# Kernel optimization log

Measured on AMD Instinct MI355X. Metric: run time of the kernel, lower is better.

The kernel has to match this reference:

```python
import jax, jax.numpy as jnp
import numpy as np

N_NODES = 50000
N_EDGES = 800000
IN_DIM = 1200   # latent_size * num_heads
OUT_DIM = 300
NEG_SLOPE = 0.2  # PyG GATConv default


def setup_inputs() -> dict:
    key = jax.random.key(0)
    k1, k2, k3, k4, k5 = jax.random.split(key, 5)
    z = jax.random.normal(k1, (N_NODES, IN_DIM), dtype=jnp.float32)
    edge_index = jax.random.randint(k2, (2, N_EDGES), 0, N_NODES, dtype=jnp.int64)
    # GATConv params (heads=1): lin weight [out, in], attention vectors [out], bias [out]
    W = jax.random.normal(k3, (OUT_DIM, IN_DIM), dtype=jnp.float32) * (1.0 / np.sqrt(IN_DIM))
    att_src = jax.random.normal(k4, (OUT_DIM,), dtype=jnp.float32) * 0.1
    att_dst = jax.random.normal(k5, (OUT_DIM,), dtype=jnp.float32) * 0.1
    bias = jnp.zeros((OUT_DIM,), dtype=jnp.float32)
    return {"z": z, "edge_index": edge_index, "W": W,
            "att_src": att_src, "att_dst": att_dst, "bias": bias}


def reference(z, edge_index, W, att_src, att_dst, bias):
    N = z.shape[0]
    # Linear projection (no bias on lin in GATConv; bias added after aggregation)
    x = z @ W.T                                   # [N, OUT_DIM]
    # add self-loops (GATConv default add_self_loops=True)
    loop = jnp.arange(N, dtype=edge_index.dtype)
    src = jnp.concatenate([edge_index[0], loop])  # message source j
    dst = jnp.concatenate([edge_index[1], loop])  # message target i
    # per-node attention logits
    a_src = x @ att_src                           # [N]
    a_dst = x @ att_dst                           # [N]
    # per-edge score, softmax over incoming edges of each target node
    e = jax.nn.leaky_relu(a_src[src] + a_dst[dst], negative_slope=NEG_SLOPE)  # [E+N]
    e_max = jax.ops.segment_max(e, dst, num_segments=N)   # every node has a self-loop
    ex = jnp.exp(e - e_max[dst])
    denom = jax.ops.segment_sum(ex, dst, num_segments=N)
    alpha = ex / denom[dst]                       # [E+N]
    # weighted aggregation (scatter-add over targets)
    out = jax.ops.segment_sum(alpha[:, None] * x[src], dst, num_segments=N)
    return out + bias
```

## Files before the change

kernel.cpp:

```cpp
#include <hip/hip_runtime.h>

#define N_NODES 50000
#define N_EDGES 800000
#define IN_DIM  1200
#define KP      1216
#define OUT_DIM 300
#define BNP     320
#define XBS     304
#define NSLOTS  (N_EDGES + N_NODES)
#define BM      96
#define GRID_M  ((N_NODES + BM - 1) / BM)

typedef __attribute__((ext_vector_type(8))) short short8;
typedef __attribute__((ext_vector_type(4))) float f32x4;

__device__ __forceinline__ short f2bf(float f) {
  unsigned u = __builtin_bit_cast(unsigned, f);
  u += 0x7fffu + ((u >> 16) & 1u);
  return (short)(u >> 16);
}
__device__ __forceinline__ float bf2f(unsigned short h) {
  return __builtin_bit_cast(float, (unsigned)h << 16);
}
__device__ __forceinline__ float lrelu(float v) { return v > 0.f ? v : 0.2f * v; }

__device__ __forceinline__ float wredMaxF(float v) {
  #pragma unroll
  for (int o = 32; o > 0; o >>= 1) v = fmaxf(v, __shfl_xor(v, o));
  return v;
}
__device__ __forceinline__ float wredSumF(float v) {
  #pragma unroll
  for (int o = 32; o > 0; o >>= 1) v += __shfl_xor(v, o);
  return v;
}

__global__ __launch_bounds__(256) void wconv(const float* __restrict__ W,
                                             unsigned short* __restrict__ Wb) {
  int f = blockIdx.x * 256 + threadIdx.x;
  if (f >= BNP * KP / 8) return;
  int n = (f * 8) / KP, c = (f * 8) % KP;
  short8 v = {0,0,0,0,0,0,0,0};
  if (n < OUT_DIM && c < IN_DIM) {
    const float4* p = reinterpret_cast<const float4*>(W + (size_t)n * IN_DIM + c);
    float4 f0 = p[0], f1 = p[1];
    v[0]=f2bf(f0.x); v[1]=f2bf(f0.y); v[2]=f2bf(f0.z); v[3]=f2bf(f0.w);
    v[4]=f2bf(f1.x); v[5]=f2bf(f1.y); v[6]=f2bf(f1.z); v[7]=f2bf(f1.w);
  }
  *reinterpret_cast<short8*>(&Wb[(size_t)n * KP + c]) = v;
}

__global__ __launch_bounds__(256, 2) void gemm_x(const float* __restrict__ z,
                                                 const unsigned short* __restrict__ Wb,
                                                 const float* __restrict__ att_s,
                                                 const float* __restrict__ att_d,
                                                 unsigned short* __restrict__ xb,
                                                 float* __restrict__ a_s,
                                                 float* __restrict__ a_d) {
  __shared__ unsigned short As[BM * 64];

  const int tid  = threadIdx.x;
  const int lane = tid & 63;
  const int wid  = tid >> 6;
  const int lr   = lane & 15;
  const int lg   = lane >> 4;
  const int m0   = blockIdx.x * BM;

  f32x4 zero4 = {0.f, 0.f, 0.f, 0.f};
  const float4 fz4 = make_float4(0.f, 0.f, 0.f, 0.f);
  f32x4 acc[6][5];
  #pragma unroll
  for (int mf = 0; mf < 6; ++mf)
    #pragma unroll
    for (int nj = 0; nj < 5; ++nj) acc[mf][nj] = zero4;

  const unsigned short* bp = Wb + (size_t)(80 * wid + lr) * KP + lg * 8;

  float4 st[3][2];
  const int srow[3] = { (tid + 0)   >> 3, (tid + 256) >> 3, (tid + 512) >> 3 };
  const int sch [3] = { (tid + 0)   & 7,  (tid + 256) & 7,  (tid + 512) & 7  };

  #define LOADST(KT)                                                          \
    _Pragma("unroll")                                                         \
    for (int j = 0; j < 3; ++j) {                                             \
      int m = m0 + srow[j], k = (KT) * 64 + sch[j] * 8;                       \
      if (m < N_NODES && k < IN_DIM) {                                        \
        const float4* p = reinterpret_cast<const float4*>(z + (size_t)m * IN_DIM + k); \
        st[j][0] = p[0]; st[j][1] = p[1];                                     \
      } else { st[j][0] = fz4; st[j][1] = fz4; }                              \
    }

  LOADST(0);

  for (int kt = 0; kt < 19; ++kt) {
    __syncthreads();
    #pragma unroll
    for (int j = 0; j < 3; ++j) {
      short8 v;
      v[0]=f2bf(st[j][0].x); v[1]=f2bf(st[j][0].y); v[2]=f2bf(st[j][0].z); v[3]=f2bf(st[j][0].w);
      v[4]=f2bf(st[j][1].x); v[5]=f2bf(st[j][1].y); v[6]=f2bf(st[j][1].z); v[7]=f2bf(st[j][1].w);
      int c2 = sch[j] ^ (srow[j] & 7);
      *reinterpret_cast<short8*>(&As[srow[j] * 64 + c2 * 8]) = v;
    }
    __syncthreads();
    if (kt < 18) { LOADST(kt + 1) }

    const unsigned short* bpk = bp + kt * 64;
    short8 bfr[5][2];
    #pragma unroll
    for (int nj = 0; nj < 5; ++nj) {
      bfr[nj][0] = *reinterpret_cast<const short8*>(bpk + (size_t)nj * 16 * KP);
      bfr[nj][1] = *reinterpret_cast<const short8*>(bpk + (size_t)nj * 16 * KP + 32);
    }

    const int sw = lr & 7;
    #pragma unroll
    for (int mf = 0; mf < 6; ++mf) {
      int arow = mf * 16 + lr;
      short8 a0 = *reinterpret_cast<const short8*>(&As[arow * 64 + ((lg    ) ^ sw) * 8]);
      short8 a1 = *reinterpret_cast<const short8*>(&As[arow * 64 + ((4 + lg) ^ sw) * 8]);
      #pragma unroll
      for (int nj = 0; nj < 5; ++nj) {
        acc[mf][nj] = __builtin_amdgcn_mfma_f32_16x16x32_bf16(a0, bfr[nj][0], acc[mf][nj], 0, 0, 0);
        acc[mf][nj] = __builtin_amdgcn_mfma_f32_16x16x32_bf16(a1, bfr[nj][1], acc[mf][nj], 0, 0, 0);
      }
    }
  }
  #undef LOADST

  __syncthreads();
  float* red = reinterpret_cast<float*>(As);

  float vs[5], vd[5];
  #pragma unroll
  for (int nj = 0; nj < 5; ++nj) {
    int c = 80 * wid + 16 * nj + lr;
    bool cv = c < OUT_DIM;
    vs[nj] = cv ? att_s[c] : 0.f;
    vd[nj] = cv ? att_d[c] : 0.f;
  }

  #pragma unroll
  for (int mf = 0; mf < 6; ++mf) {
    float ps[4] = {0.f,0.f,0.f,0.f}, pd[4] = {0.f,0.f,0.f,0.f};
    #pragma unroll
    for (int nj = 0; nj < 5; ++nj) {
      int c = 80 * wid + 16 * nj + lr;
      bool cv = c < OUT_DIM;
      #pragma unroll
      for (int jj = 0; jj < 4; ++jj) {
        float val = acc[mf][nj][jj];
        int r = m0 + 16 * mf + 4 * lg + jj;
        if (cv && r < N_NODES) xb[(size_t)r * XBS + c] = (unsigned short)f2bf(val);
        ps[jj] += val * vs[nj];
        pd[jj] += val * vd[nj];
      }
    }
    #pragma unroll
    for (int jj = 0; jj < 4; ++jj) {
      #pragma unroll
      for (int o = 8; o > 0; o >>= 1) {
        ps[jj] += __shfl_xor(ps[jj], o);
        pd[jj] += __shfl_xor(pd[jj], o);
      }
    }
    if (lr == 0) {
      #pragma unroll
      for (int jj = 0; jj < 4; ++jj) {
        int rr = 16 * mf + 4 * lg + jj;
        red[wid * 96 + rr]       = ps[jj];
        red[384 + wid * 96 + rr] = pd[jj];
      }
    }
  }
  __syncthreads();
  if (tid < 96) {
    int r = m0 + tid;
    if (r < N_NODES)
      a_s[r] = red[tid] + red[96 + tid] + red[192 + tid] + red[288 + tid];
  } else if (tid < 192) {
    int t = tid - 96, r = m0 + t;
    if (r < N_NODES)
      a_d[r] = red[384 + t] + red[384 + 96 + t] + red[384 + 192 + t] + red[384 + 288 + t];
  }
}

__global__ void hist(const int* __restrict__ ei, int* __restrict__ deg) {
  int e = blockIdx.x * blockDim.x + threadIdx.x;
  if (e < N_EDGES) {
    unsigned dst = (unsigned)ei[N_EDGES + e];
    if (dst < N_NODES) atomicAdd(&deg[dst], 1);
  }
}

#define SCAN_B 1024
#define NBLK   49

__global__ __launch_bounds__(SCAN_B) void scan1(const int* __restrict__ deg,
                                                int* __restrict__ bsum) {
  int i = blockIdx.x * SCAN_B + threadIdx.x;
  int v = (i < N_NODES) ? deg[i] + 1 : 0;
  #pragma unroll
  for (int o = 32; o > 0; o >>= 1) v += __shfl_xor(v, o);
  __shared__ int wt[16];
  if ((threadIdx.x & 63) == 0) wt[threadIdx.x >> 6] = v;
  __syncthreads();
  if (threadIdx.x == 0) {
    int t = 0;
    #pragma unroll
    for (int w = 0; w < 16; ++w) t += wt[w];
    bsum[blockIdx.x] = t;
  }
}

__global__ void scan2(const int* __restrict__ bsum, int* __restrict__ bex,
                      int* __restrict__ offs) {
  int l = threadIdx.x;
  int v = (l < NBLK) ? bsum[l] : 0;
  int incl = v;
  #pragma unroll
  for (int off = 1; off < 64; off <<= 1) {
    int u = __shfl_up(incl, off);
    if (l >= off) incl += u;
  }
  if (l < NBLK) bex[l] = incl - v;
  if (l == NBLK - 1) offs[N_NODES] = incl;
}

__global__ __launch_bounds__(SCAN_B) void scan3(const int* __restrict__ deg,
                                                const int* __restrict__ bex,
                                                int* __restrict__ offs,
                                                int* __restrict__ cursor) {
  int tid = threadIdx.x;
  int i = blockIdx.x * SCAN_B + tid;
  int lane = tid & 63, wid = tid >> 6;
  int v = (i < N_NODES) ? deg[i] + 1 : 0;
  int incl = v;
  #pragma unroll
  for (int off = 1; off < 64; off <<= 1) {
    int u = __shfl_up(incl, off);
    if (lane >= off) incl += u;
  }
  __shared__ int wt[16];
  if (lane == 63) wt[wid] = incl;
  __syncthreads();
  if (tid < 16) {
    int t = wt[tid];
    int sc = t;
    #pragma unroll
    for (int off = 1; off < 16; off <<= 1) {
      int u = __shfl_up(sc, off);
      if (tid >= off) sc += u;
    }
    wt[tid] = sc - t;
  }
  __syncthreads();
  int excl = incl - v + wt[wid] + bex[blockIdx.x];
  if (i < N_NODES) { offs[i] = excl; cursor[i] = excl; }
}

__global__ void fill(const int* __restrict__ ei, int* __restrict__ cursor,
                     int* __restrict__ srcs) {
  int e = blockIdx.x * blockDim.x + threadIdx.x;
  if (e < N_EDGES) {
    unsigned dst = (unsigned)ei[N_EDGES + e];
    unsigned src = (unsigned)ei[e];
    if (dst < N_NODES && src < N_NODES) {
      int pos = atomicAdd(&cursor[dst], 1);
      srcs[pos] = (int)src;
    }
  }
}

__global__ __launch_bounds__(256) void weights(const float* __restrict__ a_s,
                                               const float* __restrict__ a_d,
                                               const int* __restrict__ offs,
                                               const int* __restrict__ srcs,
                                               int2* __restrict__ packed) {
  int node = blockIdx.x * 4 + (threadIdx.x >> 6);
  if (node >= N_NODES) return;
  int lane = threadIdx.x & 63;
  int beg = offs[node], end = offs[node + 1];
  int ne = end - 1 - beg;
  float adi = a_d[node];
  float eself = lrelu(a_s[node] + adi);

  float m = eself;
  for (int k = lane; k < ne; k += 64)
    m = fmaxf(m, lrelu(a_s[srcs[beg + k]] + adi));
  m = wredMaxF(m);

  float s = 0.f;
  for (int k = lane; k < ne; k += 64)
    s += expf(lrelu(a_s[srcs[beg + k]] + adi) - m);
  s = wredSumF(s) + expf(eself - m);
  float inv = 1.0f / s;

  for (int k = lane; k < ne; k += 64) {
    int sj = srcs[beg + k];
    float w = expf(lrelu(a_s[sj] + adi) - m) * inv;
    packed[beg + k] = make_int2(sj, __float_as_int(w));
  }
  if (lane == 0)
    packed[end - 1] = make_int2(node, __float_as_int(expf(eself - m) * inv));
}

#define CCH 15
__global__ __launch_bounds__(256) void aggregate(const unsigned short* __restrict__ xb,
                                                 const int2* __restrict__ packed,
                                                 const int* __restrict__ offs,
                                                 const float* __restrict__ bias,
                                                 float* __restrict__ out) {
  unsigned wi = blockIdx.x * 256u + threadIdx.x;
  if (wi >= (unsigned)N_NODES * CCH) return;
  unsigned node = wi / CCH;
  unsigned cc = wi - node * CCH;

  int beg = offs[node], end = offs[node + 1];
  const unsigned short* xcol = xb + 20u * cc;

  float acc[20];
  #pragma unroll
  for (int q = 0; q < 20; ++q) acc[q] = 0.f;

  for (int k = beg; k < end; ++k) {
    int2 pw = packed[k];
    float w = __builtin_bit_cast(float, pw.y);
    const unsigned short* xr = xcol + (size_t)pw.x * XBS;
    #pragma unroll
    for (int q = 0; q < 5; ++q) {
      ushort4 xv = *reinterpret_cast<const ushort4*>(xr + 4 * q);
      acc[4*q+0] += w * bf2f(xv.x);
      acc[4*q+1] += w * bf2f(xv.y);
      acc[4*q+2] += w * bf2f(xv.z);
      acc[4*q+3] += w * bf2f(xv.w);
    }
  }
  float* op = out + (size_t)node * OUT_DIM + 20u * cc;
  const float* bp = bias + 20u * cc;
  #pragma unroll
  for (int q = 0; q < 5; ++q) {
    float4 b = *reinterpret_cast<const float4*>(bp + 4 * q);
    float4 o = {acc[4*q] + b.x, acc[4*q+1] + b.y, acc[4*q+2] + b.z, acc[4*q+3] + b.w};
    *reinterpret_cast<float4*>(op + 4 * q) = o;
  }
}

extern "C" void kernel_launch(void* const* d_in, const int* in_sizes, int n_in,
                              void* d_out, int out_size, void* d_ws, size_t ws_size,
                              hipStream_t stream) {
  const float* z     = (const float*)d_in[0];
  const int*   ei    = (const int*)d_in[1];
  const float* W     = (const float*)d_in[2];
  const float* att_s = (const float*)d_in[3];
  const float* att_d = (const float*)d_in[4];
  const float* bias  = (const float*)d_in[5];
  float* out = (float*)d_out;

  char* ws = (char*)d_ws;
  size_t off = 0;
  unsigned short* xb = (unsigned short*)(ws + off); off += (size_t)N_NODES * XBS * 2;
  unsigned short* Wb = (unsigned short*)(ws + off); off += (size_t)BNP * KP * 2;
  float* a_s  = (float*)(ws + off); off += 50048 * 4;
  float* a_d  = (float*)(ws + off); off += 50048 * 4;
  int*   deg  = (int*)(ws + off);   off += 50048 * 4;
  int*   offs = (int*)(ws + off);   off += 50056 * 4;
  int*   cur  = (int*)(ws + off);   off += 50048 * 4;
  int*   bsum = (int*)(ws + off);   off += 64 * 4;
  int*   bex  = (int*)(ws + off);   off += 64 * 4;
  int*   srcs = (int*)(ws + off);   off += (size_t)NSLOTS * 4;
  int2*  pck  = (int2*)(ws + off);  off += (size_t)NSLOTS * 8;

  (void)hipMemsetAsync(deg, 0, N_NODES * 4, stream);

  wconv<<<(BNP * KP / 8 + 255) / 256, 256, 0, stream>>>(W, Wb);
  gemm_x<<<GRID_M, 256, 0, stream>>>(z, Wb, att_s, att_d, xb, a_s, a_d);
  hist<<<(N_EDGES + 255) / 256, 256, 0, stream>>>(ei, deg);
  scan1<<<NBLK, SCAN_B, 0, stream>>>(deg, bsum);
  scan2<<<1, 64, 0, stream>>>(bsum, bex, offs);
  scan3<<<NBLK, SCAN_B, 0, stream>>>(deg, bex, offs, cur);
  fill<<<(N_EDGES + 255) / 256, 256, 0, stream>>>(ei, cur, srcs);
  weights<<<(N_NODES + 3) / 4, 256, 0, stream>>>(a_s, a_d, offs, srcs, pck);
  aggregate<<<((unsigned)N_NODES * CCH + 255) / 256, 256, 0, stream>>>(xb, pck, offs, bias, out);
}
```

Before: 363.6 us.

## Restructure projection GEMM to per-wave 32-row tiles without shared memory

The projection GEMM now gives each wave a 32-row by full 304-column tile. A operands are loaded straight from global memory into registers and double-buffered across k-steps, which removes the LDS staging and block-level barriers. The attention-logit reduction becomes wave-local, with no cross-wave shared-memory combine. In exchange each wave holds 38 accumulator fragments, which raises register pressure, and B fragments are re-read from global or L2 by every wave, so there is less reuse of W than with the shared 96-row block tile.

New measurement: 427.0 us. 17.4% more time.

```diff
diff --git a/kernel.cpp b/kernel.cpp
--- a/kernel.cpp
+++ b/kernel.cpp
@@ -8,8 +8,8 @@
 #define BNP     320
 #define XBS     304
 #define NSLOTS  (N_EDGES + N_NODES)
-#define BM      96
-#define GRID_M  ((N_NODES + BM - 1) / BM)
+#define NWAVES  ((N_NODES + 31) / 32)
+#define GEMM_GRID ((NWAVES + 3) / 4)
 
 typedef __attribute__((ext_vector_type(8))) short short8;
 typedef __attribute__((ext_vector_type(4))) float f32x4;
@@ -57,132 +57,118 @@
                                                  unsigned short* __restrict__ xb,
                                                  float* __restrict__ a_s,
                                                  float* __restrict__ a_d) {
-  __shared__ unsigned short As[BM * 64];
-
-  const int tid  = threadIdx.x;
-  const int lane = tid & 63;
-  const int wid  = tid >> 6;
-  const int lr   = lane & 15;
-  const int lg   = lane >> 4;
-  const int m0   = blockIdx.x * BM;
+  const int lane = threadIdx.x & 63;
+  const int wid  = threadIdx.x >> 6;
+  const int wg   = blockIdx.x * 4 + wid;
+  const int m0   = wg * 32;
+  if (m0 >= N_NODES) return;
+
+  const int lr = lane & 15;
+  const int lg = lane >> 4;
 
   f32x4 zero4 = {0.f, 0.f, 0.f, 0.f};
+  f32x4 acc[2][19];
+  #pragma unroll
+  for (int mf = 0; mf < 2; ++mf)
+    #pragma unroll
+    for (int t = 0; t < 19; ++t) acc[mf][t] = zero4;
+
   const float4 fz4 = make_float4(0.f, 0.f, 0.f, 0.f);
-  f32x4 acc[6][5];
-  #pragma unroll
-  for (int mf = 0; mf < 6; ++mf)
-    #pragma unroll
-    for (int nj = 0; nj < 5; ++nj) acc[mf][nj] = zero4;
-
-  const unsigned short* bp = Wb + (size_t)(80 * wid + lr) * KP + lg * 8;
-
-  float4 st[3][2];
-  const int srow[3] = { (tid + 0)   >> 3, (tid + 256) >> 3, (tid + 512) >> 3 };
-  const int sch [3] = { (tid + 0)   & 7,  (tid + 256) & 7,  (tid + 512) & 7  };
-
-  #define LOADST(KT)                                                          \
-    _Pragma("unroll")                                                         \
-    for (int j = 0; j < 3; ++j) {                                             \
-      int m = m0 + srow[j], k = (KT) * 64 + sch[j] * 8;                       \
-      if (m < N_NODES && k < IN_DIM) {                                        \
-        const float4* p = reinterpret_cast<const float4*>(z + (size_t)m * IN_DIM + k); \
-        st[j][0] = p[0]; st[j][1] = p[1];                                     \
-      } else { st[j][0] = fz4; st[j][1] = fz4; }                              \
-    }
-
-  LOADST(0);
-
-  for (int kt = 0; kt < 19; ++kt) {
-    __syncthreads();
-    #pragma unroll
-    for (int j = 0; j < 3; ++j) {
-      short8 v;
-      v[0]=f2bf(st[j][0].x); v[1]=f2bf(st[j][0].y); v[2]=f2bf(st[j][0].z); v[3]=f2bf(st[j][0].w);
-      v[4]=f2bf(st[j][1].x); v[5]=f2bf(st[j][1].y); v[6]=f2bf(st[j][1].z); v[7]=f2bf(st[j][1].w);
-      int c2 = sch[j] ^ (srow[j] & 7);
-      *reinterpret_cast<short8*>(&As[srow[j] * 64 + c2 * 8]) = v;
-    }
-    __syncthreads();
-    if (kt < 18) { LOADST(kt + 1) }
-
-    const unsigned short* bpk = bp + kt * 64;
-    short8 bfr[5][2];
-    #pragma unroll
-    for (int nj = 0; nj < 5; ++nj) {
-      bfr[nj][0] = *reinterpret_cast<const short8*>(bpk + (size_t)nj * 16 * KP);
-      bfr[nj][1] = *reinterpret_cast<const short8*>(bpk + (size_t)nj * 16 * KP + 32);
-    }
-
-    const int sw = lr & 7;
-    #pragma unroll
-    for (int mf = 0; mf < 6; ++mf) {
-      int arow = mf * 16 + lr;
-      short8 a0 = *reinterpret_cast<const short8*>(&As[arow * 64 + ((lg    ) ^ sw) * 8]);
-      short8 a1 = *reinterpret_cast<const short8*>(&As[arow * 64 + ((4 + lg) ^ sw) * 8]);
+  const int am0 = m0 + lr, am1 = m0 + 16 + lr;
+  const bool v0 = am0 < N_NODES, v1 = am1 < N_NODES;
+  const float* zp0 = z + (size_t)am0 * IN_DIM + 8 * lg;
+  const float* zp1 = z + (size_t)am1 * IN_DIM + 8 * lg;
+  const unsigned short* bp = Wb + (size_t)lr * KP + 8 * lg;
+
+  float4 sA0[2][2], sA1[2][2];
+
+  #define LOADA(ST, KS)                                                        \
+    {                                                                          \
+      int k = (KS) * 32 + 8 * lg;                                              \
+      bool kv = k < IN_DIM;                                                    \
+      if (v0 && kv) { const float4* p = reinterpret_cast<const float4*>(zp0 + (KS) * 32); \
+        ST[0][0] = p[0]; ST[0][1] = p[1]; } else { ST[0][0] = fz4; ST[0][1] = fz4; } \
+      if (v1 && kv) { const float4* p = reinterpret_cast<const float4*>(zp1 + (KS) * 32); \
+        ST[1][0] = p[0]; ST[1][1] = p[1]; } else { ST[1][0] = fz4; ST[1][1] = fz4; } \
+    }
+
+  #define STEP(ST, KS)                                                         \
+    {                                                                          \
+      short8 af0, af1;                                                         \
+      af0[0]=f2bf(ST[0][0].x); af0[1]=f2bf(ST[0][0].y); af0[2]=f2bf(ST[0][0].z); af0[3]=f2bf(ST[0][0].w); \
+      af0[4]=f2bf(ST[0][1].x); af0[5]=f2bf(ST[0][1].y); af0[6]=f2bf(ST[0][1].z); af0[7]=f2bf(ST[0][1].w); \
+      af1[0]=f2bf(ST[1][0].x); af1[1]=f2bf(ST[1][0].y); af1[2]=f2bf(ST[1][0].z); af1[3]=f2bf(ST[1][0].w); \
+      af1[4]=f2bf(ST[1][1].x); af1[5]=f2bf(ST[1][1].y); af1[6]=f2bf(ST[1][1].z); af1[7]=f2bf(ST[1][1].w); \
+      const unsigned short* bk = bp + (KS) * 32;                               \
+      {                                                                        \
+        short8 b[10];                                                          \
+        _Pragma("unroll")                                                      \
+        for (int t = 0; t < 10; ++t)                                           \
+          b[t] = *reinterpret_cast<const short8*>(bk + (size_t)t * 16 * KP);   \
+        _Pragma("unroll")                                                      \
+        for (int t = 0; t < 10; ++t) {                                         \
+          acc[0][t] = __builtin_amdgcn_mfma_f32_16x16x32_bf16(af0, b[t], acc[0][t], 0, 0, 0); \
+          acc[1][t] = __builtin_amdgcn_mfma_f32_16x16x32_bf16(af1, b[t], acc[1][t], 0, 0, 0); \
+        }                                                                      \
+      }                                                                        \
+      {                                                                        \
+        short8 b[9];                                                           \
+        _Pragma("unroll")                                                      \
+        for (int t = 0; t < 9; ++t)                                            \
+          b[t] = *reinterpret_cast<const short8*>(bk + (size_t)(t + 10) * 16 * KP); \
+        _Pragma("unroll")                                                      \
+        for (int t = 0; t < 9; ++t) {                                          \
+          acc[0][t+10] = __builtin_amdgcn_mfma_f32_16x16x32_bf16(af0, b[t], acc[0][t+10], 0, 0, 0); \
+          acc[1][t+10] = __builtin_amdgcn_mfma_f32_16x16x32_bf16(af1, b[t], acc[1][t+10], 0, 0, 0); \
+        }                                                                      \
+      }                                                                        \
+    }
+
+  LOADA(sA0, 0);
+  #pragma unroll 1
+  for (int kk = 0; kk < 19; ++kk) {
+    const int ks0 = 2 * kk, ks1 = 2 * kk + 1;
+    LOADA(sA1, ks1);
+    STEP(sA0, ks0);
+    if (kk < 18) { LOADA(sA0, ks0 + 2); }
+    STEP(sA1, ks1);
+  }
+  #undef LOADA
+  #undef STEP
+
+  float ps[2][4] = {{0,0,0,0},{0,0,0,0}}, pd[2][4] = {{0,0,0,0},{0,0,0,0}};
+  #pragma unroll
+  for (int t = 0; t < 19; ++t) {
+    int c = 16 * t + lr;
+    bool cv = c < OUT_DIM;
+    float vs = cv ? att_s[c] : 0.f;
+    float vd = cv ? att_d[c] : 0.f;
+    #pragma unroll
+    for (int mf = 0; mf < 2; ++mf) {
       #pragma unroll
-      for (int nj = 0; nj < 5; ++nj) {
-        acc[mf][nj] = __builtin_amdgcn_mfma_f32_16x16x32_bf16(a0, bfr[nj][0], acc[mf][nj], 0, 0, 0);
-        acc[mf][nj] = __builtin_amdgcn_mfma_f32_16x16x32_bf16(a1, bfr[nj][1], acc[mf][nj], 0, 0, 0);
+      for (int j = 0; j < 4; ++j) {
+        float val = acc[mf][t][j];
+        int r = m0 + 16 * mf + 4 * lg + j;
+        if (cv && r < N_NODES) xb[(size_t)r * XBS + c] = (unsigned short)f2bf(val);
+        ps[mf][j] += val * vs;
+        pd[mf][j] += val * vd;
       }
     }
   }
-  #undef LOADST
-
-  __syncthreads();
-  float* red = reinterpret_cast<float*>(As);
-
-  float vs[5], vd[5];
-  #pragma unroll
-  for (int nj = 0; nj < 5; ++nj) {
-    int c = 80 * wid + 16 * nj + lr;
-    bool cv = c < OUT_DIM;
-    vs[nj] = cv ? att_s[c] : 0.f;
-    vd[nj] = cv ? att_d[c] : 0.f;
-  }
-
-  #pragma unroll
-  for (int mf = 0; mf < 6; ++mf) {
-    float ps[4] = {0.f,0.f,0.f,0.f}, pd[4] = {0.f,0.f,0.f,0.f};
-    #pragma unroll
-    for (int nj = 0; nj < 5; ++nj) {
-      int c = 80 * wid + 16 * nj + lr;
-      bool cv = c < OUT_DIM;
-      #pragma unroll
-      for (int jj = 0; jj < 4; ++jj) {
-        float val = acc[mf][nj][jj];
-        int r = m0 + 16 * mf + 4 * lg + jj;
-        if (cv && r < N_NODES) xb[(size_t)r * XBS + c] = (unsigned short)f2bf(val);
-        ps[jj] += val * vs[nj];
-        pd[jj] += val * vd[nj];
-      }
-    }
-    #pragma unroll
-    for (int jj = 0; jj < 4; ++jj) {
+  #pragma unroll
+  for (int mf = 0; mf < 2; ++mf)
+    #pragma unroll
+    for (int j = 0; j < 4; ++j) {
       #pragma unroll
       for (int o = 8; o > 0; o >>= 1) {
-        ps[jj] += __shfl_xor(ps[jj], o);
-        pd[jj] += __shfl_xor(pd[jj], o);
+        ps[mf][j] += __shfl_xor(ps[mf][j], o);
+        pd[mf][j] += __shfl_xor(pd[mf][j], o);
       }
-    }
-    if (lr == 0) {
-      #pragma unroll
-      for (int jj = 0; jj < 4; ++jj) {
-        int rr = 16 * mf + 4 * lg + jj;
-        red[wid * 96 + rr]       = ps[jj];
-        red[384 + wid * 96 + rr] = pd[jj];
+      if (lr == 0) {
+        int r = m0 + 16 * mf + 4 * lg + j;
+        if (r < N_NODES) { a_s[r] = ps[mf][j]; a_d[r] = pd[mf][j]; }
       }
     }
-  }
-  __syncthreads();
-  if (tid < 96) {
-    int r = m0 + tid;
-    if (r < N_NODES)
-      a_s[r] = red[tid] + red[96 + tid] + red[192 + tid] + red[288 + tid];
-  } else if (tid < 192) {
-    int t = tid - 96, r = m0 + t;
-    if (r < N_NODES)
-      a_d[r] = red[384 + t] + red[384 + 96 + t] + red[384 + 192 + t] + red[384 + 288 + t];
-  }
 }
 
 __global__ void hist(const int* __restrict__ ei, int* __restrict__ deg) {
@@ -374,7 +360,7 @@
   (void)hipMemsetAsync(deg, 0, N_NODES * 4, stream);
 
   wconv<<<(BNP * KP / 8 + 255) / 256, 256, 0, stream>>>(W, Wb);
-  gemm_x<<<GRID_M, 256, 0, stream>>>(z, Wb, att_s, att_d, xb, a_s, a_d);
+  gemm_x<<<GEMM_GRID, 256, 0, stream>>>(z, Wb, att_s, att_d, xb, a_s, a_d);
   hist<<<(N_EDGES + 255) / 256, 256, 0, stream>>>(ei, deg);
   scan1<<<NBLK, SCAN_B, 0, stream>>>(deg, bsum);
   scan2<<<1, 64, 0, stream>>>(bsum, bex, offs);
```

## Halve GEMM row tile, double-buffer LDS staging, raise occupancy to three blocks

Applied to the files above, without the earlier changes.

The projection GEMM tile drops from 96 to 48 rows, and the A-tile staging moves to two LDS buffers so the next tile's global load and bf16 conversion overlap the current MFMA work with one barrier per step. Staging now uses float4 loads with 4-wide bf16 stores, and launch bounds ask for three blocks per CU. The aim is better latency hiding and more blocks across the CUs. The cost is that each W fragment is reused across fewer rows, so global/L2 traffic for W per output roughly doubles.

Result: slower. 397.2 us (+9.2%).

```diff
diff --git a/kernel.cpp b/kernel.cpp
--- a/kernel.cpp
+++ b/kernel.cpp
@@ -8,10 +8,11 @@
 #define BNP     320
 #define XBS     304
 #define NSLOTS  (N_EDGES + N_NODES)
-#define BM      96
+#define BM      48
 #define GRID_M  ((N_NODES + BM - 1) / BM)
 
 typedef __attribute__((ext_vector_type(8))) short short8;
+typedef __attribute__((ext_vector_type(4))) short short4v;
 typedef __attribute__((ext_vector_type(4))) float f32x4;
 
 __device__ __forceinline__ short f2bf(float f) {
@@ -50,14 +51,14 @@
   *reinterpret_cast<short8*>(&Wb[(size_t)n * KP + c]) = v;
 }
 
-__global__ __launch_bounds__(256, 2) void gemm_x(const float* __restrict__ z,
+__global__ __launch_bounds__(256, 3) void gemm_x(const float* __restrict__ z,
                                                  const unsigned short* __restrict__ Wb,
                                                  const float* __restrict__ att_s,
                                                  const float* __restrict__ att_d,
                                                  unsigned short* __restrict__ xb,
                                                  float* __restrict__ a_s,
                                                  float* __restrict__ a_d) {
-  __shared__ unsigned short As[BM * 64];
+  __shared__ unsigned short As[2][BM * 64];
 
   const int tid  = threadIdx.x;
   const int lane = tid & 63;
@@ -68,68 +69,93 @@
 
   f32x4 zero4 = {0.f, 0.f, 0.f, 0.f};
   const float4 fz4 = make_float4(0.f, 0.f, 0.f, 0.f);
-  f32x4 acc[6][5];
-  #pragma unroll
-  for (int mf = 0; mf < 6; ++mf)
+  f32x4 acc[3][5];
+  #pragma unroll
+  for (int mf = 0; mf < 3; ++mf)
     #pragma unroll
     for (int nj = 0; nj < 5; ++nj) acc[mf][nj] = zero4;
 
-  const unsigned short* bp = Wb + (size_t)(80 * wid + lr) * KP + lg * 8;
-
-  float4 st[3][2];
-  const int srow[3] = { (tid + 0)   >> 3, (tid + 256) >> 3, (tid + 512) >> 3 };
-  const int sch [3] = { (tid + 0)   & 7,  (tid + 256) & 7,  (tid + 512) & 7  };
-
-  #define LOADST(KT)                                                          \
-    _Pragma("unroll")                                                         \
-    for (int j = 0; j < 3; ++j) {                                             \
-      int m = m0 + srow[j], k = (KT) * 64 + sch[j] * 8;                       \
-      if (m < N_NODES && k < IN_DIM) {                                        \
-        const float4* p = reinterpret_cast<const float4*>(z + (size_t)m * IN_DIM + k); \
-        st[j][0] = p[0]; st[j][1] = p[1];                                     \
-      } else { st[j][0] = fz4; st[j][1] = fz4; }                              \
+  const unsigned short* bp = Wb + (size_t)(80 * wid + lr) * KP + 8 * lg;
+
+  const int srow_[3] = { (tid      ) >> 4, (tid + 256) >> 4, (tid + 512) >> 4 };
+  const int sf4c_[3] = { (tid      ) & 15, (tid + 256) & 15, (tid + 512) & 15 };
+  float4 sg[3];
+
+  #define LOADST(KT)                                                           \
+    _Pragma("unroll")                                                          \
+    for (int q = 0; q < 3; ++q) {                                              \
+      int m = m0 + srow_[q];                                                   \
+      int k = (KT) * 64 + sf4c_[q] * 4;                                        \
+      sg[q] = (m < N_NODES && k < IN_DIM)                                      \
+        ? *reinterpret_cast<const float4*>(z + (size_t)m * IN_DIM + k)         \
+        : fz4;                                                                 \
+    }
+
+  #define WRITEST(BUF)                                                         \
+    _Pragma("unroll")                                                          \
+    for (int q = 0; q < 3; ++q) {                                              \
+      short4v v;                                                               \
+      v[0]=f2bf(sg[q].x); v[1]=f2bf(sg[q].y); v[2]=f2bf(sg[q].z); v[3]=f2bf(sg[q].w); \
+      int row = srow_[q], f4c = sf4c_[q];                                      \
+      int c2 = (f4c >> 1) ^ (row & 7);                                         \
+      *reinterpret_cast<short4v*>(&As[BUF][row * 64 + c2 * 8 + (f4c & 1) * 4]) = v; \
     }
 
   LOADST(0);
-
+  WRITEST(0);
+  __syncthreads();
+
+  #pragma unroll 1
   for (int kt = 0; kt < 19; ++kt) {
-    __syncthreads();
-    #pragma unroll
-    for (int j = 0; j < 3; ++j) {
-      short8 v;
-      v[0]=f2bf(st[j][0].x); v[1]=f2bf(st[j][0].y); v[2]=f2bf(st[j][0].z); v[3]=f2bf(st[j][0].w);
-      v[4]=f2bf(st[j][1].x); v[5]=f2bf(st[j][1].y); v[6]=f2bf(st[j][1].z); v[7]=f2bf(st[j][1].w);
-      int c2 = sch[j] ^ (srow[j] & 7);
-      *reinterpret_cast<short8*>(&As[srow[j] * 64 + c2 * 8]) = v;
-    }
-    __syncthreads();
-    if (kt < 18) { LOADST(kt + 1) }
+    const int cur = kt & 1;
+    if (kt < 18) { LOADST(kt + 1); }
 
     const unsigned short* bpk = bp + kt * 64;
-    short8 bfr[5][2];
-    #pragma unroll
-    for (int nj = 0; nj < 5; ++nj) {
-      bfr[nj][0] = *reinterpret_cast<const short8*>(bpk + (size_t)nj * 16 * KP);
-      bfr[nj][1] = *reinterpret_cast<const short8*>(bpk + (size_t)nj * 16 * KP + 32);
-    }
-
-    const int sw = lr & 7;
-    #pragma unroll
-    for (int mf = 0; mf < 6; ++mf) {
-      int arow = mf * 16 + lr;
-      short8 a0 = *reinterpret_cast<const short8*>(&As[arow * 64 + ((lg    ) ^ sw) * 8]);
-      short8 a1 = *reinterpret_cast<const short8*>(&As[arow * 64 + ((4 + lg) ^ sw) * 8]);
-      #pragma unroll
-      for (int nj = 0; nj < 5; ++nj) {
-        acc[mf][nj] = __builtin_amdgcn_mfma_f32_16x16x32_bf16(a0, bfr[nj][0], acc[mf][nj], 0, 0, 0);
-        acc[mf][nj] = __builtin_amdgcn_mfma_f32_16x16x32_bf16(a1, bfr[nj][1], acc[mf][nj], 0, 0, 0);
+    #pragma unroll
+    for (int ks = 0; ks < 2; ++ks) {
+      const unsigned short* bk = bpk + ks * 32;
+      short8 b0 = *reinterpret_cast<const short8*>(bk);
+      short8 b1 = *reinterpret_cast<const short8*>(bk + (size_t)16 * KP);
+      short8 b2 = *reinterpret_cast<const short8*>(bk + (size_t)32 * KP);
+      short8 b3 = *reinterpret_cast<const short8*>(bk + (size_t)48 * KP);
+      short8 b4 = *reinterpret_cast<const short8*>(bk + (size_t)64 * KP);
+      const int ch = ks * 4 + lg;
+      short8 a0, a1, a2;
+      {
+        int r0 = lr,      c0 = (ch ^ (r0 & 7));
+        int r1 = 16 + lr, c1 = (ch ^ (r1 & 7));
+        int r2 = 32 + lr, c2 = (ch ^ (r2 & 7));
+        a0 = *reinterpret_cast<const short8*>(&As[cur][r0 * 64 + c0 * 8]);
+        a1 = *reinterpret_cast<const short8*>(&As[cur][r1 * 64 + c1 * 8]);
+        a2 = *reinterpret_cast<const short8*>(&As[cur][r2 * 64 + c2 * 8]);
       }
+      acc[0][0] = __builtin_amdgcn_mfma_f32_16x16x32_bf16(a0, b0, acc[0][0], 0, 0, 0);
+      acc[1][0] = __builtin_amdgcn_mfma_f32_16x16x32_bf16(a1, b0, acc[1][0], 0, 0, 0);
+      acc[2][0] = __builtin_amdgcn_mfma_f32_16x16x32_bf16(a2, b0, acc[2][0], 0, 0, 0);
+      acc[0][1] = __builtin_amdgcn_mfma_f32_16x16x32_bf16(a0, b1, acc[0][1], 0, 0, 0);
+      acc[1][1] = __builtin_amdgcn_mfma_f32_16x16x32_bf16(a1, b1, acc[1][1], 0, 0, 0);
+      acc[2][1] = __builtin_amdgcn_mfma_f32_16x16x32_bf16(a2, b1, acc[2][1], 0, 0, 0);
+      acc[0][2] = __builtin_amdgcn_mfma_f32_16x16x32_bf16(a0, b2, acc[0][2], 0, 0, 0);
+      acc[1][2] = __builtin_amdgcn_mfma_f32_16x16x32_bf16(a1, b2, acc[1][2], 0, 0, 0);
+      acc[2][2] = __builtin_amdgcn_mfma_f32_16x16x32_bf16(a2, b2, acc[2][2], 0, 0, 0);
+      acc[0][3] = __builtin_amdgcn_mfma_f32_16x16x32_bf16(a0, b3, acc[0][3], 0, 0, 0);
+      acc[1][3] = __builtin_amdgcn_mfma_f32_16x16x32_bf16(a1, b3, acc[1][3], 0, 0, 0);
+      acc[2][3] = __builtin_amdgcn_mfma_f32_16x16x32_bf16(a2, b3, acc[2][3], 0, 0, 0);
+      acc[0][4] = __builtin_amdgcn_mfma_f32_16x16x32_bf16(a0, b4, acc[0][4], 0, 0, 0);
+      acc[1][4] = __builtin_amdgcn_mfma_f32_16x16x32_bf16(a1, b4, acc[1][4], 0, 0, 0);
+      acc[2][4] = __builtin_amdgcn_mfma_f32_16x16x32_bf16(a2, b4, acc[2][4], 0, 0, 0);
+    }
+
+    if (kt < 18) {
+      WRITEST(cur ^ 1);
+      __syncthreads();
     }
   }
   #undef LOADST
-
-  __syncthreads();
-  float* red = reinterpret_cast<float*>(As);
+  #undef WRITEST
+
+  __syncthreads();
+  float* red = reinterpret_cast<float*>(&As[0][0]);
 
   float vs[5], vd[5];
   #pragma unroll
@@ -141,7 +167,7 @@
   }
 
   #pragma unroll
-  for (int mf = 0; mf < 6; ++mf) {
+  for (int mf = 0; mf < 3; ++mf) {
     float ps[4] = {0.f,0.f,0.f,0.f}, pd[4] = {0.f,0.f,0.f,0.f};
     #pragma unroll
     for (int nj = 0; nj < 5; ++nj) {
@@ -168,20 +194,20 @@
       #pragma unroll
       for (int jj = 0; jj < 4; ++jj) {
         int rr = 16 * mf + 4 * lg + jj;
-        red[wid * 96 + rr]       = ps[jj];
-        red[384 + wid * 96 + rr] = pd[jj];
+        red[wid * 48 + rr]       = ps[jj];
+        red[192 + wid * 48 + rr] = pd[jj];
       }
     }
   }
   __syncthreads();
-  if (tid < 96) {
+  if (tid < 48) {
     int r = m0 + tid;
     if (r < N_NODES)
-      a_s[r] = red[tid] + red[96 + tid] + red[192 + tid] + red[288 + tid];
-  } else if (tid < 192) {
-    int t = tid - 96, r = m0 + t;
+      a_s[r] = red[tid] + red[48 + tid] + red[96 + tid] + red[144 + tid];
+  } else if (tid < 96) {
+    int t = tid - 48, r = m0 + t;
     if (r < N_NODES)
-      a_d[r] = red[384 + t] + red[384 + 96 + t] + red[384 + 192 + t] + red[384 + 288 + t];
+      a_d[r] = red[192 + t] + red[192 + 48 + t] + red[192 + 96 + t] + red[192 + 144 + t];
   }
 }
 
```

## Retile GEMM with LDS double-buffering; recompute attention weights in aggregate

Applied to the files above, without the earlier changes.

The projection GEMM moves from 96-row tiles, with B fragments read straight from global memory, to 64-row tiles. Both A and B are now staged in double-buffered swizzled LDS with a k-step of 32, and the 4 waves are split 2x2. The edge-weight kernel no longer writes packed (src, weight) pairs. It stores only the per-node max and inverse sum, and aggregate recomputes each edge weight from a_s/a_d and handles the self-loop separately. The CSR scan drops the self-loop slot. This cuts 8-byte-per-edge writes and reads, but adds redundant exp and a_s gathers in each of the 15 column-chunk threads per node. The GEMM also re-reads W per block via LDS with a different occupancy profile.

Result: faster. 333.1 us (-8.4%).

```diff
diff --git a/kernel.cpp b/kernel.cpp
--- a/kernel.cpp
+++ b/kernel.cpp
@@ -7,8 +7,8 @@
 #define OUT_DIM 300
 #define BNP     320
 #define XBS     304
-#define NSLOTS  (N_EDGES + N_NODES)
-#define BM      96
+#define BM      64
+#define NKT     38
 #define GRID_M  ((N_NODES + BM - 1) / BM)
 
 typedef __attribute__((ext_vector_type(8))) short short8;
@@ -50,138 +50,145 @@
   *reinterpret_cast<short8*>(&Wb[(size_t)n * KP + c]) = v;
 }
 
-__global__ __launch_bounds__(256, 2) void gemm_x(const float* __restrict__ z,
-                                                 const unsigned short* __restrict__ Wb,
-                                                 const float* __restrict__ att_s,
-                                                 const float* __restrict__ att_d,
-                                                 unsigned short* __restrict__ xb,
-                                                 float* __restrict__ a_s,
-                                                 float* __restrict__ a_d) {
-  __shared__ unsigned short As[BM * 64];
+__global__ __launch_bounds__(256) void gemm_x(const float* __restrict__ z,
+                                              const unsigned short* __restrict__ Wb,
+                                              const float* __restrict__ att_s,
+                                              const float* __restrict__ att_d,
+                                              unsigned short* __restrict__ xb,
+                                              float* __restrict__ a_s,
+                                              float* __restrict__ a_d) {
+  __shared__ __align__(16) unsigned short As[2][BM * 32];
+  __shared__ __align__(16) unsigned short Bs[2][BNP * 32];
 
   const int tid  = threadIdx.x;
   const int lane = tid & 63;
   const int wid  = tid >> 6;
   const int lr   = lane & 15;
   const int lg   = lane >> 4;
+  const int mw   = wid >> 1;
+  const int nw   = wid & 1;
   const int m0   = blockIdx.x * BM;
 
   f32x4 zero4 = {0.f, 0.f, 0.f, 0.f};
   const float4 fz4 = make_float4(0.f, 0.f, 0.f, 0.f);
-  f32x4 acc[6][5];
-  #pragma unroll
-  for (int mf = 0; mf < 6; ++mf)
-    #pragma unroll
-    for (int nj = 0; nj < 5; ++nj) acc[mf][nj] = zero4;
-
-  const unsigned short* bp = Wb + (size_t)(80 * wid + lr) * KP + lg * 8;
-
-  float4 st[3][2];
-  const int srow[3] = { (tid + 0)   >> 3, (tid + 256) >> 3, (tid + 512) >> 3 };
-  const int sch [3] = { (tid + 0)   & 7,  (tid + 256) & 7,  (tid + 512) & 7  };
-
-  #define LOADST(KT)                                                          \
-    _Pragma("unroll")                                                         \
-    for (int j = 0; j < 3; ++j) {                                             \
-      int m = m0 + srow[j], k = (KT) * 64 + sch[j] * 8;                       \
-      if (m < N_NODES && k < IN_DIM) {                                        \
-        const float4* p = reinterpret_cast<const float4*>(z + (size_t)m * IN_DIM + k); \
-        st[j][0] = p[0]; st[j][1] = p[1];                                     \
-      } else { st[j][0] = fz4; st[j][1] = fz4; }                              \
-    }
-
-  LOADST(0);
-
-  for (int kt = 0; kt < 19; ++kt) {
-    __syncthreads();
-    #pragma unroll
-    for (int j = 0; j < 3; ++j) {
-      short8 v;
-      v[0]=f2bf(st[j][0].x); v[1]=f2bf(st[j][0].y); v[2]=f2bf(st[j][0].z); v[3]=f2bf(st[j][0].w);
-      v[4]=f2bf(st[j][1].x); v[5]=f2bf(st[j][1].y); v[6]=f2bf(st[j][1].z); v[7]=f2bf(st[j][1].w);
-      int c2 = sch[j] ^ (srow[j] & 7);
-      *reinterpret_cast<short8*>(&As[srow[j] * 64 + c2 * 8]) = v;
-    }
-    __syncthreads();
-    if (kt < 18) { LOADST(kt + 1) }
-
-    const unsigned short* bpk = bp + kt * 64;
-    short8 bfr[5][2];
-    #pragma unroll
-    for (int nj = 0; nj < 5; ++nj) {
-      bfr[nj][0] = *reinterpret_cast<const short8*>(bpk + (size_t)nj * 16 * KP);
-      bfr[nj][1] = *reinterpret_cast<const short8*>(bpk + (size_t)nj * 16 * KP + 32);
-    }
-
-    const int sw = lr & 7;
-    #pragma unroll
-    for (int mf = 0; mf < 6; ++mf) {
-      int arow = mf * 16 + lr;
-      short8 a0 = *reinterpret_cast<const short8*>(&As[arow * 64 + ((lg    ) ^ sw) * 8]);
-      short8 a1 = *reinterpret_cast<const short8*>(&As[arow * 64 + ((4 + lg) ^ sw) * 8]);
-      #pragma unroll
-      for (int nj = 0; nj < 5; ++nj) {
-        acc[mf][nj] = __builtin_amdgcn_mfma_f32_16x16x32_bf16(a0, bfr[nj][0], acc[mf][nj], 0, 0, 0);
-        acc[mf][nj] = __builtin_amdgcn_mfma_f32_16x16x32_bf16(a1, bfr[nj][1], acc[mf][nj], 0, 0, 0);
-      }
-    }
-  }
-  #undef LOADST
-
+  f32x4 acc[2][10];
+  #pragma unroll
+  for (int mf = 0; mf < 2; ++mf)
+    #pragma unroll
+    for (int nj = 0; nj < 10; ++nj) acc[mf][nj] = zero4;
+
+  const int ra = tid >> 2, ca = tid & 3;
+  const int am = m0 + ra;
+  float4 ga0, ga1;
+  short8 gb[5];
+
+  #define LOADAB(KT)                                                          \
+    {                                                                         \
+      int k = (KT) * 32 + ca * 8;                                             \
+      if (am < N_NODES && k < IN_DIM) {                                       \
+        const float4* p = reinterpret_cast<const float4*>(z + (size_t)am * IN_DIM + k); \
+        ga0 = p[0]; ga1 = p[1];                                               \
+      } else { ga0 = fz4; ga1 = fz4; }                                        \
+      _Pragma("unroll")                                                       \
+      for (int j = 0; j < 5; ++j) {                                           \
+        int s = tid + 256 * j;                                                \
+        gb[j] = *reinterpret_cast<const short8*>(                             \
+            Wb + (size_t)(s >> 2) * KP + (KT) * 32 + (s & 3) * 8);            \
+      }                                                                       \
+    }
+
+  #define WRITEST(BUF)                                                        \
+    {                                                                         \
+      short8 v;                                                               \
+      v[0]=f2bf(ga0.x); v[1]=f2bf(ga0.y); v[2]=f2bf(ga0.z); v[3]=f2bf(ga0.w); \
+      v[4]=f2bf(ga1.x); v[5]=f2bf(ga1.y); v[6]=f2bf(ga1.z); v[7]=f2bf(ga1.w); \
+      int c2a = ca ^ ((ra >> 2) & 3);                                         \
+      *reinterpret_cast<short8*>(&As[BUF][ra * 32 + c2a * 8]) = v;            \
+      _Pragma("unroll")                                                       \
+      for (int j = 0; j < 5; ++j) {                                           \
+        int s = tid + 256 * j;                                                \
+        int rb = s >> 2, cb = s & 3;                                          \
+        int c2b = cb ^ ((rb >> 2) & 3);                                       \
+        *reinterpret_cast<short8*>(&Bs[BUF][rb * 32 + c2b * 8]) = gb[j];      \
+      }                                                                       \
+    }
+
+  LOADAB(0);
+  WRITEST(0);
   __syncthreads();
-  float* red = reinterpret_cast<float*>(As);
-
-  float vs[5], vd[5];
-  #pragma unroll
-  for (int nj = 0; nj < 5; ++nj) {
-    int c = 80 * wid + 16 * nj + lr;
+
+  #pragma unroll 1
+  for (int kt = 0; kt < NKT; ++kt) {
+    const int cur = kt & 1;
+    if (kt < NKT - 1) { LOADAB(kt + 1); }
+
+    short8 a0, a1;
+    {
+      int r0 = mw * 32 + lr,      ch0 = lg ^ ((r0 >> 2) & 3);
+      int r1 = mw * 32 + 16 + lr, ch1 = lg ^ ((r1 >> 2) & 3);
+      a0 = *reinterpret_cast<const short8*>(&As[cur][r0 * 32 + ch0 * 8]);
+      a1 = *reinterpret_cast<const short8*>(&As[cur][r1 * 32 + ch1 * 8]);
+    }
+    #pragma unroll
+    for (int nj = 0; nj < 10; ++nj) {
+      int rb = nw * 160 + nj * 16 + lr;
+      int ch = lg ^ ((rb >> 2) & 3);
+      short8 b = *reinterpret_cast<const short8*>(&Bs[cur][rb * 32 + ch * 8]);
+      acc[0][nj] = __builtin_amdgcn_mfma_f32_16x16x32_bf16(a0, b, acc[0][nj], 0, 0, 0);
+      acc[1][nj] = __builtin_amdgcn_mfma_f32_16x16x32_bf16(a1, b, acc[1][nj], 0, 0, 0);
+    }
+
+    if (kt < NKT - 1) {
+      WRITEST(cur ^ 1);
+      __syncthreads();
+    }
+  }
+  #undef LOADAB
+  #undef WRITEST
+
+  float* red = reinterpret_cast<float*>(&As[0][0]);
+
+  float ps[2][4] = {{0,0,0,0},{0,0,0,0}}, pd[2][4] = {{0,0,0,0},{0,0,0,0}};
+  #pragma unroll
+  for (int nj = 0; nj < 10; ++nj) {
+    int c = nw * 160 + nj * 16 + lr;
     bool cv = c < OUT_DIM;
-    vs[nj] = cv ? att_s[c] : 0.f;
-    vd[nj] = cv ? att_d[c] : 0.f;
-  }
-
-  #pragma unroll
-  for (int mf = 0; mf < 6; ++mf) {
-    float ps[4] = {0.f,0.f,0.f,0.f}, pd[4] = {0.f,0.f,0.f,0.f};
-    #pragma unroll
-    for (int nj = 0; nj < 5; ++nj) {
-      int c = 80 * wid + 16 * nj + lr;
-      bool cv = c < OUT_DIM;
+    float vs = cv ? att_s[c] : 0.f;
+    float vd = cv ? att_d[c] : 0.f;
+    #pragma unroll
+    for (int mf = 0; mf < 2; ++mf) {
       #pragma unroll
       for (int jj = 0; jj < 4; ++jj) {
         float val = acc[mf][nj][jj];
-        int r = m0 + 16 * mf + 4 * lg + jj;
+        int r = m0 + mw * 32 + mf * 16 + 4 * lg + jj;
         if (cv && r < N_NODES) xb[(size_t)r * XBS + c] = (unsigned short)f2bf(val);
-        ps[jj] += val * vs[nj];
-        pd[jj] += val * vd[nj];
+        ps[mf][jj] += val * vs;
+        pd[mf][jj] += val * vd;
       }
     }
+  }
+  #pragma unroll
+  for (int mf = 0; mf < 2; ++mf)
     #pragma unroll
     for (int jj = 0; jj < 4; ++jj) {
       #pragma unroll
       for (int o = 8; o > 0; o >>= 1) {
-        ps[jj] += __shfl_xor(ps[jj], o);
-        pd[jj] += __shfl_xor(pd[jj], o);
+        ps[mf][jj] += __shfl_xor(ps[mf][jj], o);
+        pd[mf][jj] += __shfl_xor(pd[mf][jj], o);
       }
-    }
-    if (lr == 0) {
-      #pragma unroll
-      for (int jj = 0; jj < 4; ++jj) {
-        int rr = 16 * mf + 4 * lg + jj;
-        red[wid * 96 + rr]       = ps[jj];
-        red[384 + wid * 96 + rr] = pd[jj];
+      if (lr == 0) {
+        int rr = mw * 32 + mf * 16 + 4 * lg + jj;
+        red[nw * 64 + rr]       = ps[mf][jj];
+        red[128 + nw * 64 + rr] = pd[mf][jj];
       }
     }
-  }
   __syncthreads();
-  if (tid < 96) {
+  if (tid < 64) {
     int r = m0 + tid;
-    if (r < N_NODES)
-      a_s[r] = red[tid] + red[96 + tid] + red[192 + tid] + red[288 + tid];
-  } else if (tid < 192) {
-    int t = tid - 96, r = m0 + t;
-    if (r < N_NODES)
-      a_d[r] = red[384 + t] + red[384 + 96 + t] + red[384 + 192 + t] + red[384 + 288 + t];
+    if (r < N_NODES) a_s[r] = red[tid] + red[64 + tid];
+  } else if (tid < 128) {
+    int t = tid - 64, r = m0 + t;
+    if (r < N_NODES) a_d[r] = red[128 + t] + red[192 + t];
   }
 }
 
@@ -199,7 +206,7 @@
 __global__ __launch_bounds__(SCAN_B) void scan1(const int* __restrict__ deg,
                                                 int* __restrict__ bsum) {
   int i = blockIdx.x * SCAN_B + threadIdx.x;
-  int v = (i < N_NODES) ? deg[i] + 1 : 0;
+  int v = (i < N_NODES) ? deg[i] : 0;
   #pragma unroll
   for (int o = 32; o > 0; o >>= 1) v += __shfl_xor(v, o);
   __shared__ int wt[16];
@@ -234,7 +241,7 @@
   int tid = threadIdx.x;
   int i = blockIdx.x * SCAN_B + tid;
   int lane = tid & 63, wid = tid >> 6;
-  int v = (i < N_NODES) ? deg[i] + 1 : 0;
+  int v = (i < N_NODES) ? deg[i] : 0;
   int incl = v;
   #pragma unroll
   for (int off = 1; off < 64; off <<= 1) {
@@ -272,43 +279,37 @@
   }
 }
 
-__global__ __launch_bounds__(256) void weights(const float* __restrict__ a_s,
-                                               const float* __restrict__ a_d,
-                                               const int* __restrict__ offs,
-                                               const int* __restrict__ srcs,
-                                               int2* __restrict__ packed) {
+__global__ __launch_bounds__(256) void minv_k(const float* __restrict__ a_s,
+                                              const float* __restrict__ a_d,
+                                              const int* __restrict__ offs,
+                                              const int* __restrict__ srcs,
+                                              float2* __restrict__ minv) {
   int node = blockIdx.x * 4 + (threadIdx.x >> 6);
   if (node >= N_NODES) return;
   int lane = threadIdx.x & 63;
   int beg = offs[node], end = offs[node + 1];
-  int ne = end - 1 - beg;
   float adi = a_d[node];
   float eself = lrelu(a_s[node] + adi);
 
   float m = eself;
-  for (int k = lane; k < ne; k += 64)
-    m = fmaxf(m, lrelu(a_s[srcs[beg + k]] + adi));
+  for (int k = beg + lane; k < end; k += 64)
+    m = fmaxf(m, lrelu(a_s[srcs[k]] + adi));
   m = wredMaxF(m);
 
   float s = 0.f;
-  for (int k = lane; k < ne; k += 64)
-    s += expf(lrelu(a_s[srcs[beg + k]] + adi) - m);
+  for (int k = beg + lane; k < end; k += 64)
+    s += expf(lrelu(a_s[srcs[k]] + adi) - m);
   s = wredSumF(s) + expf(eself - m);
-  float inv = 1.0f / s;
-
-  for (int k = lane; k < ne; k += 64) {
-    int sj = srcs[beg + k];
-    float w = expf(lrelu(a_s[sj] + adi) - m) * inv;
-    packed[beg + k] = make_int2(sj, __float_as_int(w));
-  }
-  if (lane == 0)
-    packed[end - 1] = make_int2(node, __float_as_int(expf(eself - m) * inv));
+  if (lane == 0) minv[node] = make_float2(m, 1.0f / s);
 }
 
 #define CCH 15
 __global__ __launch_bounds__(256) void aggregate(const unsigned short* __restrict__ xb,
-                                                 const int2* __restrict__ packed,
+                                                 const float* __restrict__ a_s,
+                                                 const float* __restrict__ a_d,
+                                                 const float2* __restrict__ minv,
                                                  const int* __restrict__ offs,
+                                                 const int* __restrict__ srcs,
                                                  const float* __restrict__ bias,
                                                  float* __restrict__ out) {
   unsigned wi = blockIdx.x * 256u + threadIdx.x;
@@ -317,16 +318,30 @@
   unsigned cc = wi - node * CCH;
 
   int beg = offs[node], end = offs[node + 1];
+  float2 mi = minv[node];
+  const float m = mi.x, inv = mi.y;
+  const float adi = a_d[node];
+  const float wself = expf(lrelu(a_s[node] + adi) - m) * inv;
+
   const unsigned short* xcol = xb + 20u * cc;
 
   float acc[20];
-  #pragma unroll
-  for (int q = 0; q < 20; ++q) acc[q] = 0.f;
+  {
+    const unsigned short* xr = xcol + (size_t)node * XBS;
+    #pragma unroll
+    for (int q = 0; q < 5; ++q) {
+      ushort4 xv = *reinterpret_cast<const ushort4*>(xr + 4 * q);
+      acc[4*q+0] = wself * bf2f(xv.x);
+      acc[4*q+1] = wself * bf2f(xv.y);
+      acc[4*q+2] = wself * bf2f(xv.z);
+      acc[4*q+3] = wself * bf2f(xv.w);
+    }
+  }
 
   for (int k = beg; k < end; ++k) {
-    int2 pw = packed[k];
-    float w = __builtin_bit_cast(float, pw.y);
-    const unsigned short* xr = xcol + (size_t)pw.x * XBS;
+    int sj = srcs[k];
+    float w = expf(lrelu(a_s[sj] + adi) - m) * inv;
+    const unsigned short* xr = xcol + (size_t)sj * XBS;
     #pragma unroll
     for (int q = 0; q < 5; ++q) {
       ushort4 xv = *reinterpret_cast<const ushort4*>(xr + 4 * q);
@@ -361,15 +376,15 @@
   size_t off = 0;
   unsigned short* xb = (unsigned short*)(ws + off); off += (size_t)N_NODES * XBS * 2;
   unsigned short* Wb = (unsigned short*)(ws + off); off += (size_t)BNP * KP * 2;
-  float* a_s  = (float*)(ws + off); off += 50048 * 4;
-  float* a_d  = (float*)(ws + off); off += 50048 * 4;
-  int*   deg  = (int*)(ws + off);   off += 50048 * 4;
-  int*   offs = (int*)(ws + off);   off += 50056 * 4;
-  int*   cur  = (int*)(ws + off);   off += 50048 * 4;
-  int*   bsum = (int*)(ws + off);   off += 64 * 4;
-  int*   bex  = (int*)(ws + off);   off += 64 * 4;
-  int*   srcs = (int*)(ws + off);   off += (size_t)NSLOTS * 4;
-  int2*  pck  = (int2*)(ws + off);  off += (size_t)NSLOTS * 8;
+  float*  a_s  = (float*)(ws + off);  off += 50048 * 4;
+  float*  a_d  = (float*)(ws + off);  off += 50048 * 4;
+  int*    deg  = (int*)(ws + off);    off += 50048 * 4;
+  int*    offs = (int*)(ws + off);    off += 50056 * 4;
+  int*    cur  = (int*)(ws + off);    off += 50048 * 4;
+  int*    bsum = (int*)(ws + off);    off += 64 * 4;
+  int*    bex  = (int*)(ws + off);    off += 64 * 4;
+  int*    srcs = (int*)(ws + off);    off += (size_t)N_EDGES * 4;
+  float2* minv = (float2*)(ws + off); off += (size_t)50048 * 8;
 
   (void)hipMemsetAsync(deg, 0, N_NODES * 4, stream);
 
@@ -380,6 +395,7 @@
   scan2<<<1, 64, 0, stream>>>(bsum, bex, offs);
   scan3<<<NBLK, SCAN_B, 0, stream>>>(deg, bex, offs, cur);
   fill<<<(N_EDGES + 255) / 256, 256, 0, stream>>>(ei, cur, srcs);
-  weights<<<(N_NODES + 3) / 4, 256, 0, stream>>>(a_s, a_d, offs, srcs, pck);
-  aggregate<<<((unsigned)N_NODES * CCH + 255) / 256, 256, 0, stream>>>(xb, pck, offs, bias, out);
-}
+  minv_k<<<(N_NODES + 3) / 4, 256, 0, stream>>>(a_s, a_d, offs, srcs, minv);
+  aggregate<<<((unsigned)N_NODES * CCH + 255) / 256, 256, 0, stream>>>(
+      xb, a_s, a_d, minv, offs, srcs, bias, out);
+}
```
